# Performance work log

Measured on AMD Instinct MI355X. Metric: run time of the kernel, lower is better.

## Reference

```python
import jax, jax.numpy as jnp
from jax import lax
import numpy as np

D_MODEL, D_STATE, D_CONV, EXPAND = 512, 16, 4, 2
D_INNER = EXPAND * D_MODEL
B_SZ, SEQ = 16, 2048


def setup_inputs() -> dict:
    key = jax.random.key(0)
    ks = jax.random.split(key, 8)
    s = 0.02
    x = jax.random.normal(ks[0], (B_SZ, SEQ, D_MODEL), jnp.float32)
    W_in = jax.random.normal(ks[1], (2 * D_INNER, D_MODEL), jnp.float32) * s
    conv_w = jax.random.normal(ks[2], (D_INNER, 1, D_CONV), jnp.float32) * s
    conv_b = jnp.zeros((D_INNER,), jnp.float32)
    W_x = jax.random.normal(ks[3], (2 * D_STATE, D_INNER), jnp.float32) * s
    W_dt = jax.random.normal(ks[4], (D_INNER, D_INNER), jnp.float32) * s
    b_dt = jnp.zeros((D_INNER,), jnp.float32)
    # A_log = -logspace(log10(0.001), log10(1.0), d_state), exactly as in source
    A_log = jnp.asarray(-np.logspace(np.log10(0.001), 0.0, D_STATE), jnp.float32)
    D = jnp.ones((D_INNER,), jnp.float32) * 0.1
    W_out = jax.random.normal(ks[5], (D_MODEL, D_INNER), jnp.float32) * s
    ln_g = jnp.ones((D_MODEL,), jnp.float32)
    ln_b = jnp.zeros((D_MODEL,), jnp.float32)
    return dict(x=x, W_in=W_in, conv_w=conv_w, conv_b=conv_b, W_x=W_x,
                W_dt=W_dt, b_dt=b_dt, A_log=A_log, D=D, W_out=W_out,
                ln_g=ln_g, ln_b=ln_b)


def _selective_scan(u, delta, A, B, C, Dp):
    # u, delta: [b, s, di]; B, C: [b, s, ds]; A: [ds]; Dp: [di]
    def step(state, inp):
        d_t, u_t, B_t, C_t = inp            # [b,di],[b,di],[b,ds],[b,ds]
        dA = jnp.exp(jnp.clip(d_t[:, :, None] * A[None, None, :], -5.0, 5.0))
        dBu = (d_t * u_t)[:, :, None] * B_t[:, None, :]
        state = dA * state + dBu            # [b,di,ds]
        y_t = jnp.einsum('bds,bs->bd', state, C_t)
        return state, y_t

    b = u.shape[0]
    init = jnp.zeros((b, D_INNER, D_STATE), u.dtype)
    xs = (delta.transpose(1, 0, 2), u.transpose(1, 0, 2),
          B.transpose(1, 0, 2), C.transpose(1, 0, 2))
    _, ys = lax.scan(step, init, xs)        # [s, b, di]
    return ys.transpose(1, 0, 2) + u * Dp


def reference(x, W_in, conv_w, conv_b, W_x, W_dt, b_dt, A_log, D, W_out, ln_g, ln_b):
    x = jnp.clip(x, -10.0, 10.0)
    x_and_res = x @ W_in.T                  # [b, s, 2*di]
    x_p, res = jnp.split(x_and_res, 2, axis=-1)
    # causal depthwise conv1d (left pad d_conv-1, truncate to seq_len)
    xc = lax.conv_general_dilated(
        x_p.transpose(0, 2, 1), conv_w, window_strides=(1,),
        padding=[(D_CONV - 1, 0)], dimension_numbers=('NCH', 'OIH', 'NCH'),
        feature_group_count=D_INNER)
    xc = (xc + conv_b[None, :, None]).transpose(0, 2, 1)  # [b, s, di]
    xc = jax.nn.silu(xc)
    ssm = xc @ W_x.T                        # [b, s, 2*ds]
    Bm, Cm = jnp.split(ssm, 2, axis=-1)
    dt = xc @ W_dt.T + b_dt                 # [b, s, di]
    y = _selective_scan(xc, dt, A_log, Bm, Cm, D)
    y = y * jax.nn.silu(res)
    out = y @ W_out.T + x
    # LayerNorm (eps=1e-5)
    mu = out.mean(-1, keepdims=True)
    var = ((out - mu) ** 2).mean(-1, keepdims=True)
    return (out - mu) * lax.rsqrt(var + 1e-5) * ln_g + ln_b
```

## Files before the change

### kernel.cpp

```cpp
#include <hip/hip_runtime.h>
#include <hip/hip_bf16.h>
#include <math.h>

#define B_SZ 16
#define SEQ 2048
#define D_MODEL 512
#define D_INNER 1024
#define D_STATE 16
#define D_CONV 4
#define NSEG 64
#define SEGLEN (SEQ / NSEG)
#define LOG2E 1.44269504f

typedef __attribute__((ext_vector_type(8))) short short8;
typedef __attribute__((ext_vector_type(4))) float f32x4;
typedef const __attribute__((address_space(1))) void* gas_ptr;
typedef __attribute__((address_space(3))) void* las_ptr;

__device__ __forceinline__ float bf2f(unsigned int bits16) {
    union { unsigned int i; float f; } v; v.i = bits16 << 16; return v.f;
}
__device__ __forceinline__ unsigned short f2bf(float f) {
    union { float f; unsigned int i; } v; v.f = f;
    unsigned int r = v.i + 0x7FFFu + ((v.i >> 16) & 1u);
    return (unsigned short)(r >> 16);
}
__device__ __forceinline__ void async_g2l(const void* g, void* l) {
    __builtin_amdgcn_global_load_lds((gas_ptr)g, (las_ptr)l, 16, 0, 0);
}
__device__ __forceinline__ float fast_exp2(float x) { return __builtin_amdgcn_exp2f(x); }
__device__ __forceinline__ float fast_rcp(float x)  { return __builtin_amdgcn_rcpf(x); }
__device__ __forceinline__ float clamp3(float x, float lo, float hi) {
    return __builtin_amdgcn_fmed3f(x, lo, hi);
}
__device__ __forceinline__ float silu(float x) {
    return x * fast_rcp(1.f + fast_exp2(-x * LOG2E));
}
__device__ __forceinline__ void vm_wait0() { asm volatile("s_waitcnt vmcnt(0)" ::: "memory"); }
__device__ __forceinline__ void vm_wait3() { asm volatile("s_waitcnt vmcnt(3)" ::: "memory"); }
__device__ __forceinline__ void vm_wait4() { asm volatile("s_waitcnt vmcnt(4)" ::: "memory"); }

__global__ __launch_bounds__(256) void cast_bf16(
    const float4* __restrict__ in, ushort4* __restrict__ out, int n4, int do_clip)
{
    int i = blockIdx.x * 256 + threadIdx.x;
    if (i >= n4) return;
    float4 v = in[i];
    if (do_clip) {
        v.x = clamp3(v.x, -10.f, 10.f);
        v.y = clamp3(v.y, -10.f, 10.f);
        v.z = clamp3(v.z, -10.f, 10.f);
        v.w = clamp3(v.w, -10.f, 10.f);
    }
    ushort4 o;
    o.x = f2bf(v.x); o.y = f2bf(v.y); o.z = f2bf(v.z); o.w = f2bf(v.w);
    out[i] = o;
}

__global__ __launch_bounds__(512, 4) void gemm_big(
    const unsigned short* __restrict__ A, const unsigned short* __restrict__ Bw,
    void* __restrict__ C, int K, int ldc, int nbn_shift,
    const float* __restrict__ bias,
    const float* __restrict__ add, int ldadd, int clip_add, int out_bf16)
{
    __shared__ unsigned short As[3][256][32];
    __shared__ unsigned short Bs[3][128][32];
    const int h = blockIdx.x;
    const int xk = h & 7;
    const int qb = h >> 3;
    const int bn = (qb & ((1 << nbn_shift) - 1)) * 128;
    const int bm = ((qb >> nbn_shift) * 8 + xk) * 256;
    const int tid = threadIdx.x;
    const int wv = tid >> 6;
    const int l  = tid & 63;
    const int lr = l >> 2;
    const int lc = l & 3;
    const int wm = (wv >> 1) * 64;
    const int wn = (wv & 1) * 64;
    const int r16 = l & 15;
    const int q   = l >> 4;
    const int gsw = (lc - ((lr >> 1) & 3)) & 3;
    const int ssw = ((q + ((r16 >> 1) & 3)) & 3) * 8;

    f32x4 acc[4][4];
    #pragma unroll
    for (int i = 0; i < 4; i++)
        #pragma unroll
        for (int j = 0; j < 4; j++)
            acc[i][j] = (f32x4){0.f, 0.f, 0.f, 0.f};

#define STAGEB(kk, bb) { \
        const int k0_ = (kk) * 32; \
        _Pragma("unroll") \
        for (int p_ = 0; p_ < 2; p_++) { \
            const int arow_ = wv * 32 + p_ * 16 + lr; \
            async_g2l((const char*)A + (((size_t)(bm + arow_)) * K + k0_ + gsw * 8) * 2, \
                      (char*)&As[bb][wv * 32 + p_ * 16][0]); \
        } \
        const int brow_ = wv * 16 + lr; \
        async_g2l((const char*)Bw + (((size_t)(bn + brow_)) * K + k0_ + gsw * 8) * 2, \
                  (char*)&Bs[bb][wv * 16][0]); \
    }

    const int nk = K >> 5;
    STAGEB(0, 0);
    STAGEB(1, 1);
    int c0 = 0, c1 = 1, c2 = 2;

    for (int kk = 0; kk < nk; kk++) {
        if (kk + 1 < nk) vm_wait3(); else vm_wait0();
        __builtin_amdgcn_s_barrier();

        short8 af[4], bfv[4];
        #pragma unroll
        for (int i = 0; i < 4; i++) {
            af[i]  = *(const short8*)&As[c0][wm + i * 16 + r16][ssw];
            bfv[i] = *(const short8*)&Bs[c0][wn + i * 16 + r16][ssw];
        }
        if (kk + 2 < nk) STAGEB(kk + 2, c2);

        #pragma unroll
        for (int i = 0; i < 4; i++)
            #pragma unroll
            for (int j = 0; j < 4; j++)
                acc[i][j] = __builtin_amdgcn_mfma_f32_16x16x32_bf16(
                    af[i], bfv[j], acc[i][j], 0, 0, 0);

        int t = c0; c0 = c1; c1 = c2; c2 = t;
    }
#undef STAGEB

    #pragma unroll
    for (int i = 0; i < 4; i++) {
        #pragma unroll
        for (int rr = 0; rr < 4; rr++) {
            int m = bm + wm + i * 16 + q * 4 + rr;
            #pragma unroll
            for (int j = 0; j < 4; j++) {
                int n = bn + wn + j * 16 + r16;
                float v = acc[i][j][rr];
                if (bias) v += bias[n];
                if (add) {
                    float a = add[(size_t)m * ldadd + n];
                    if (clip_add) a = clamp3(a, -10.f, 10.f);
                    v += a;
                }
                if (out_bf16)
                    ((unsigned short*)C)[(size_t)m * ldc + n] = f2bf(v);
                else
                    ((float*)C)[(size_t)m * ldc + n] = v;
            }
        }
    }
}

__global__ __launch_bounds__(256) void gemm_bf16(
    const unsigned short* __restrict__ A, const unsigned short* __restrict__ Bw,
    void* __restrict__ C, int K, int ldc, int nbn_shift,
    const float* __restrict__ bias,
    const float* __restrict__ add, int ldadd, int clip_add, int out_bf16)
{
    __shared__ unsigned short As[3][128][32];
    __shared__ unsigned short Bs[3][128][32];
    const int h = blockIdx.x;
    const int xk = h & 7;
    const int qb = h >> 3;
    const int bn = (qb & ((1 << nbn_shift) - 1)) * 128;
    const int bm = ((qb >> nbn_shift) * 8 + xk) * 128;
    const int tid = threadIdx.x;
    const int wv = tid >> 6;
    const int l  = tid & 63;
    const int lr = l >> 2;
    const int lc = l & 3;
    const int wm = (wv >> 1) * 64;
    const int wn = (wv & 1) * 64;
    const int r16 = l & 15;
    const int q   = l >> 4;
    const int gsw = (lc - ((lr >> 1) & 3)) & 3;
    const int ssw = ((q + ((r16 >> 1) & 3)) & 3) * 8;

    f32x4 acc[4][4];
    #pragma unroll
    for (int i = 0; i < 4; i++)
        #pragma unroll
        for (int j = 0; j < 4; j++)
            acc[i][j] = (f32x4){0.f, 0.f, 0.f, 0.f};

#define STAGE(kk, bb) { \
        const int k0_ = (kk) * 32; \
        _Pragma("unroll") \
        for (int p_ = 0; p_ < 2; p_++) { \
            const int row_ = wv * 32 + p_ * 16 + lr; \
            async_g2l((const char*)A + (((size_t)(bm + row_)) * K + k0_ + gsw * 8) * 2, \
                      (char*)&As[bb][wv * 32 + p_ * 16][0]); \
            async_g2l((const char*)Bw + (((size_t)(bn + row_)) * K + k0_ + gsw * 8) * 2, \
                      (char*)&Bs[bb][wv * 32 + p_ * 16][0]); \
        } }

    const int nk = K >> 5;
    STAGE(0, 0);
    STAGE(1, 1);
    int c0 = 0, c1 = 1, c2 = 2;

    for (int kk = 0; kk < nk; kk++) {
        if (kk + 1 < nk) vm_wait4(); else vm_wait0();
        __builtin_amdgcn_s_barrier();

        short8 af[4], bfv[4];
        #pragma unroll
        for (int i = 0; i < 4; i++) {
            af[i]  = *(const short8*)&As[c0][wm + i * 16 + r16][ssw];
            bfv[i] = *(const short8*)&Bs[c0][wn + i * 16 + r16][ssw];
        }
        if (kk + 2 < nk) STAGE(kk + 2, c2);

        #pragma unroll
        for (int i = 0; i < 4; i++)
            #pragma unroll
            for (int j = 0; j < 4; j++)
                acc[i][j] = __builtin_amdgcn_mfma_f32_16x16x32_bf16(
                    af[i], bfv[j], acc[i][j], 0, 0, 0);

        int t = c0; c0 = c1; c1 = c2; c2 = t;
    }
#undef STAGE

    #pragma unroll
    for (int i = 0; i < 4; i++) {
        #pragma unroll
        for (int rr = 0; rr < 4; rr++) {
            int m = bm + wm + i * 16 + q * 4 + rr;
            #pragma unroll
            for (int j = 0; j < 4; j++) {
                int n = bn + wn + j * 16 + r16;
                float v = acc[i][j][rr];
                if (bias) v += bias[n];
                if (add) {
                    float a = add[(size_t)m * ldadd + n];
                    if (clip_add) a = clamp3(a, -10.f, 10.f);
                    v += a;
                }
                if (out_bf16)
                    ((unsigned short*)C)[(size_t)m * ldc + n] = f2bf(v);
                else
                    ((float*)C)[(size_t)m * ldc + n] = v;
            }
        }
    }
}

__global__ __launch_bounds__(256) void gemm_bc(
    const unsigned short* __restrict__ A, const unsigned short* __restrict__ Bw,
    float* __restrict__ C)
{
    const int tid = threadIdx.x;
    const int wv  = tid >> 6;
    const int l   = tid & 63;
    const int r16 = l & 15;
    const int q   = l >> 4;
    const int row0 = blockIdx.x * 64 + wv * 16;

    const unsigned short* ap  = A  + (size_t)(row0 + r16) * 1024 + q * 8;
    const unsigned short* bp0 = Bw + (size_t)r16 * 1024 + q * 8;
    const unsigned short* bp1 = Bw + (size_t)(16 + r16) * 1024 + q * 8;

    f32x4 acc0 = {0.f, 0.f, 0.f, 0.f}, acc1 = {0.f, 0.f, 0.f, 0.f};
    #pragma unroll 4
    for (int k = 0; k < 1024; k += 32) {
        short8 af = *(const short8*)(ap + k);
        short8 b0 = *(const short8*)(bp0 + k);
        short8 b1 = *(const short8*)(bp1 + k);
        acc0 = __builtin_amdgcn_mfma_f32_16x16x32_bf16(af, b0, acc0, 0, 0, 0);
        acc1 = __builtin_amdgcn_mfma_f32_16x16x32_bf16(af, b1, acc1, 0, 0, 0);
    }
    #pragma unroll
    for (int rr = 0; rr < 4; rr++) {
        int m = row0 + q * 4 + rr;
        C[(size_t)m * 32 + r16]      = acc0[rr];
        C[(size_t)m * 32 + 16 + r16] = acc1[rr];
    }
}

__global__ __launch_bounds__(256) void conv_silu(
    const unsigned short* __restrict__ xp, const float* __restrict__ cw,
    const float* __restrict__ cb, unsigned short* __restrict__ xc)
{
    int idx = blockIdx.x * 256 + threadIdx.x;
    int c4 = (idx & 255) << 2;
    int bt = idx >> 8;
    int t  = bt & (SEQ - 1);

    float4 acc = *(const float4*)(cb + c4);
    float4 w0 = *(const float4*)(cw + (c4 + 0) * 4);
    float4 w1 = *(const float4*)(cw + (c4 + 1) * 4);
    float4 w2 = *(const float4*)(cw + (c4 + 2) * 4);
    float4 w3 = *(const float4*)(cw + (c4 + 3) * 4);

    #pragma unroll
    for (int k = 0; k < D_CONV; k++) {
        int tt = t - (D_CONV - 1) + k;
        if (tt >= 0) {
            ushort4 xv = *(const ushort4*)(xp + (size_t)(bt - (D_CONV - 1) + k) * 2048 + c4);
            acc.x += bf2f(xv.x) * ((const float*)&w0)[k];
            acc.y += bf2f(xv.y) * ((const float*)&w1)[k];
            acc.z += bf2f(xv.z) * ((const float*)&w2)[k];
            acc.w += bf2f(xv.w) * ((const float*)&w3)[k];
        }
    }
    ushort4 o;
    o.x = f2bf(silu(acc.x));
    o.y = f2bf(silu(acc.y));
    o.z = f2bf(silu(acc.z));
    o.w = f2bf(silu(acc.w));
    *(ushort4*)(xc + (size_t)bt * 1024 + c4) = o;
}

__global__ __launch_bounds__(64, 4) void scan_phaseA(
    const unsigned short* __restrict__ xpres, const float* __restrict__ BC,
    const unsigned short* __restrict__ xc, const float* __restrict__ A_log,
    float* __restrict__ stA, float* __restrict__ prA)
{
    __shared__ float bc_lds[SEGLEN][32];
    const int bx = blockIdx.x;
    const int seg = bx & (NSEG - 1);
    const int dg  = (bx >> 6) & 15;
    const int b   = bx >> 10;
    if (seg == NSEG - 1) return;
    const int lane = threadIdx.x;
    const int d = dg * 64 + lane;
    const float CL = 5.f * LOG2E;

    const size_t rowbase = (size_t)b * SEQ + (size_t)seg * SEGLEN;
    const float* BCp = BC + rowbase * 32;

    #pragma unroll
    for (int c = 0; c < 4; c++)
        async_g2l(BCp + c * 256 + lane * 4,
                  (char*)&bc_lds[0][0] + c * 1024 + lane * 16);

    float A2[16];
    #pragma unroll
    for (int n = 0; n < 16; n++) A2[n] = A_log[n] * LOG2E;

    const unsigned short* dtp = xpres + rowbase * 2048 + d;
    const unsigned short* up  = xc + rowbase * 1024 + d;

    float st[16] = {};
    float se[16] = {};
    unsigned short dta[4], dtb[4], ua[4], ub[4];

#define LOADGA(g, dt_, u_) { \
        _Pragma("unroll") for (int jj = 0; jj < 4; ++jj) { \
            const int t_ = (g) * 4 + jj; \
            dt_[jj] = dtp[(size_t)t_ * 2048]; \
            u_[jj]  = up[(size_t)t_ * 1024]; \
        } }

#define COMPGA(g, dt_, u_) { \
        _Pragma("unroll") for (int jj = 0; jj < 4; ++jj) { \
            const int t_ = (g) * 4 + jj; \
            const float dtv_ = bf2f(dt_[jj]); \
            const float du_ = dtv_ * bf2f(u_[jj]); \
            float Bv_[16]; \
            _Pragma("unroll") for (int n = 0; n < 4; ++n) \
                *(float4*)&Bv_[n * 4] = *(const float4*)&bc_lds[t_][n * 4]; \
            _Pragma("unroll") for (int n = 0; n < 16; ++n) { \
                const float e_ = clamp3(dtv_ * A2[n], -CL, CL); \
                se[n] += e_; \
                st[n] = fast_exp2(e_) * st[n] + du_ * Bv_[n]; \
            } } }

    LOADGA(0, dta, ua);
    __syncthreads();

    for (int g = 0; g < 8; g += 2) {
        LOADGA(g + 1, dtb, ub);
        COMPGA(g, dta, ua);
        if (g + 2 < 8) LOADGA(g + 2, dta, ua);
        COMPGA(g + 1, dtb, ub);
    }
#undef LOADGA
#undef COMPGA

    size_t o = (((size_t)b * NSEG + seg) * 1024 + d) * 16;
    #pragma unroll
    for (int n4 = 0; n4 < 4; n4++) {
        *(float4*)(stA + o + n4 * 4) = *(float4*)&st[n4 * 4];
        float4 pv;
        pv.x = fast_exp2(clamp3(se[n4 * 4 + 0], -115.41f, 115.41f));
        pv.y = fast_exp2(clamp3(se[n4 * 4 + 1], -115.41f, 115.41f));
        pv.z = fast_exp2(clamp3(se[n4 * 4 + 2], -115.41f, 115.41f));
        pv.w = fast_exp2(clamp3(se[n4 * 4 + 3], -115.41f, 115.41f));
        *(float4*)(prA + o + n4 * 4) = pv;
    }
}

__global__ __launch_bounds__(256) void scan_combine(
    float* __restrict__ stA, const float* __restrict__ prA, int total)
{
    int idx = blockIdx.x * 256 + threadIdx.x;
    if (idx >= total) return;
    int dn = idx & 16383;
    int b  = idx >> 14;
    float prev = 0.f;
    #pragma unroll 4
    for (int s = 0; s < NSEG; s++) {
        size_t o = ((size_t)b * NSEG + s) * 16384 + dn;
        float a = stA[o], pr = prA[o];
        stA[o] = prev;
        prev = a + pr * prev;
    }
}

__global__ __launch_bounds__(64, 4) void scan_phaseC(
    const unsigned short* __restrict__ xpres, const float* __restrict__ BC,
    const unsigned short* __restrict__ xc, const float* __restrict__ A_log,
    const float* __restrict__ Dvec, const float* __restrict__ stIn,
    unsigned short* __restrict__ y_bf)
{
    __shared__ float bc_lds[SEGLEN][32];
    const int bx = blockIdx.x;
    const int seg = bx & (NSEG - 1);
    const int dg  = (bx >> 6) & 15;
    const int b   = bx >> 10;
    const int lane = threadIdx.x;
    const int d = dg * 64 + lane;
    const float CL = 5.f * LOG2E;

    const size_t rowbase = (size_t)b * SEQ + (size_t)seg * SEGLEN;
    const float* BCp = BC + rowbase * 32;

    #pragma unroll
    for (int c = 0; c < 4; c++)
        async_g2l(BCp + c * 256 + lane * 4,
                  (char*)&bc_lds[0][0] + c * 1024 + lane * 16);

    float A2[16];
    #pragma unroll
    for (int n = 0; n < 16; n++) A2[n] = A_log[n] * LOG2E;
    const float Dp = Dvec[d];

    const unsigned short* dtp  = xpres + rowbase * 2048 + d;
    const unsigned short* resp = xpres + rowbase * 2048 + 1024 + d;
    const unsigned short* up   = xc + rowbase * 1024 + d;
    unsigned short* yp = y_bf + rowbase * 1024 + d;

    float st[16];
    size_t o = (((size_t)b * NSEG + seg) * 1024 + d) * 16;
    #pragma unroll
    for (int n4 = 0; n4 < 4; n4++)
        *(float4*)&st[n4 * 4] = *(const float4*)(stIn + o + n4 * 4);

    unsigned short dta[4], dtb[4], ua[4], ub[4], ra[4], rb[4];

#define LOADGC(g, dt_, r_, u_) { \
        _Pragma("unroll") for (int jj = 0; jj < 4; ++jj) { \
            const int t_ = (g) * 4 + jj; \
            dt_[jj] = dtp[(size_t)t_ * 2048]; \
            r_[jj]  = resp[(size_t)t_ * 2048]; \
            u_[jj]  = up[(size_t)t_ * 1024]; \
        } }

#define COMPGC(g, dt_, r_, u_) { \
        _Pragma("unroll") for (int jj = 0; jj < 4; ++jj) { \
            const int t_ = (g) * 4 + jj; \
            const float dtv_ = bf2f(dt_[jj]); \
            const float uu_ = bf2f(u_[jj]); \
            const float du_ = dtv_ * uu_; \
            float V_[16]; \
            _Pragma("unroll") for (int n = 0; n < 4; ++n) \
                *(float4*)&V_[n * 4] = *(const float4*)&bc_lds[t_][n * 4]; \
            _Pragma("unroll") for (int n = 0; n < 16; ++n) { \
                const float e_ = clamp3(dtv_ * A2[n], -CL, CL); \
                st[n] = fast_exp2(e_) * st[n] + du_ * V_[n]; \
            } \
            _Pragma("unroll") for (int n = 0; n < 4; ++n) \
                *(float4*)&V_[n * 4] = *(const float4*)&bc_lds[t_][16 + n * 4]; \
            float y_ = 0.f; \
            _Pragma("unroll") for (int n = 0; n < 16; ++n) \
                y_ += st[n] * V_[n]; \
            const float outv_ = (y_ + uu_ * Dp) * silu(bf2f(r_[jj])); \
            yp[(size_t)t_ * 1024] = f2bf(outv_); \
        } }

    LOADGC(0, dta, ra, ua);
    __syncthreads();

    for (int g = 0; g < 8; g += 2) {
        LOADGC(g + 1, dtb, rb, ub);
        COMPGC(g, dta, ra, ua);
        if (g + 2 < 8) LOADGC(g + 2, dta, ra, ua);
        COMPGC(g + 1, dtb, rb, ub);
    }
#undef LOADGC
#undef COMPGC
}

__global__ __launch_bounds__(128) void ln_kernel(
    float* __restrict__ out, const float* __restrict__ g,
    const float* __restrict__ bta)
{
    const int row = blockIdx.x;
    float* p = out + (size_t)row * D_MODEL;
    const int tid = threadIdx.x;

    float4 v = ((const float4*)p)[tid];
    float s1 = v.x + v.y + v.z + v.w;
    float s2 = v.x * v.x + v.y * v.y + v.z * v.z + v.w * v.w;
    #pragma unroll
    for (int off = 32; off > 0; off >>= 1) {
        s1 += __shfl_xor(s1, off);
        s2 += __shfl_xor(s2, off);
    }
    __shared__ float r1[2], r2[2];
    if ((tid & 63) == 0) { r1[tid >> 6] = s1; r2[tid >> 6] = s2; }
    __syncthreads();
    s1 = r1[0] + r1[1];
    s2 = r2[0] + r2[1];

    const float mu  = s1 * (1.f / D_MODEL);
    const float var = s2 * (1.f / D_MODEL) - mu * mu;
    const float rstd = rsqrtf(var + 1e-5f);

    float4 gg = ((const float4*)g)[tid];
    float4 bb = ((const float4*)bta)[tid];
    float4 o;
    o.x = (v.x - mu) * rstd * gg.x + bb.x;
    o.y = (v.y - mu) * rstd * gg.y + bb.y;
    o.z = (v.z - mu) * rstd * gg.z + bb.z;
    o.w = (v.w - mu) * rstd * gg.w + bb.w;
    ((float4*)p)[tid] = o;
}

extern "C" void kernel_launch(void* const* d_in, const int* in_sizes, int n_in,
                              void* d_out, int out_size, void* d_ws, size_t ws_size,
                              hipStream_t stream)
{
    const float* x      = (const float*)d_in[0];
    const float* W_in   = (const float*)d_in[1];
    const float* conv_w = (const float*)d_in[2];
    const float* conv_b = (const float*)d_in[3];
    const float* W_x    = (const float*)d_in[4];
    const float* W_dt   = (const float*)d_in[5];
    const float* b_dt   = (const float*)d_in[6];
    const float* A_log  = (const float*)d_in[7];
    const float* Dv     = (const float*)d_in[8];
    const float* W_out  = (const float*)d_in[9];
    const float* ln_g   = (const float*)d_in[10];
    const float* ln_b   = (const float*)d_in[11];
    float* out = (float*)d_out;

    const size_t szWin  = (size_t)2048 * 512;
    const size_t szWdt  = (size_t)1024 * 1024;
    const size_t szWout = (size_t)512 * 1024;
    const size_t szWx   = (size_t)32 * 1024;
    char* p = (char*)d_ws;
    unsigned short* Wib  = (unsigned short*)p; p += szWin * 2;
    unsigned short* Wdtb = (unsigned short*)p; p += szWdt * 2;
    unsigned short* Wob  = (unsigned short*)p; p += szWout * 2;
    unsigned short* Wxb  = (unsigned short*)p; p += szWx * 2;
    const size_t fixed_bytes = (size_t)(p - (char*)d_ws);

    const size_t per_batch =
        (size_t)SEQ * 2048 * 2
      + (size_t)SEQ * 1024 * 2
      + (size_t)SEQ * 1024 * 2
      + (size_t)SEQ * 32 * 4
      + (size_t)2 * NSEG * 1024 * 16 * 4;
    int cb = 16;
    while (cb > 1 && fixed_bytes + (size_t)cb * per_batch > ws_size) cb >>= 1;
    const int Mc = cb * SEQ;

    unsigned short* xpres = (unsigned short*)p; p += (size_t)Mc * 2048 * 2;
    unsigned short* ybuf  = (unsigned short*)p; p += (size_t)Mc * 1024 * 2;
    unsigned short* x_bf  = ybuf;
    unsigned short* xc_bf = (unsigned short*)p; p += (size_t)Mc * 1024 * 2;
    float*          BCb   = (float*)p;          p += (size_t)Mc * 32 * 4;
    float*          stA   = (float*)p;          p += (size_t)cb * NSEG * 16384 * 4;
    float*          prA   = (float*)p;

    cast_bf16<<<(int)(szWin / 4 + 255) / 256, 256, 0, stream>>>((const float4*)W_in,  (ushort4*)Wib,  (int)(szWin / 4), 0);
    cast_bf16<<<(int)(szWdt / 4 + 255) / 256, 256, 0, stream>>>((const float4*)W_dt,  (ushort4*)Wdtb, (int)(szWdt / 4), 0);
    cast_bf16<<<(int)(szWout / 4 + 255) / 256, 256, 0, stream>>>((const float4*)W_out, (ushort4*)Wob, (int)(szWout / 4), 0);
    cast_bf16<<<(int)(szWx / 4 + 255) / 256, 256, 0, stream>>>((const float4*)W_x,   (ushort4*)Wxb,  (int)(szWx / 4), 0);

    for (int b0 = 0; b0 < B_SZ; b0 += cb) {
        const float* xk   = x   + (size_t)b0 * SEQ * D_MODEL;
        float*       outk = out + (size_t)b0 * SEQ * D_MODEL;

        cast_bf16<<<(Mc * 512 / 4) / 256, 256, 0, stream>>>(
            (const float4*)xk, (ushort4*)x_bf, Mc * 512 / 4, 1);

        gemm_big<<<16 * (Mc / 256), 512, 0, stream>>>(
            x_bf, Wib, xpres, 512, 2048, 4, nullptr, nullptr, 0, 0, 1);

        conv_silu<<<Mc, 256, 0, stream>>>(xpres, conv_w, conv_b, xc_bf);

        gemm_bc<<<Mc / 64, 256, 0, stream>>>(xc_bf, Wxb, BCb);

        gemm_big<<<8 * (Mc / 256), 512, 0, stream>>>(
            xc_bf, Wdtb, xpres, 1024, 2048, 3, b_dt, nullptr, 0, 0, 1);

        scan_phaseA<<<cb * NSEG * 16, 64, 0, stream>>>(xpres, BCb, xc_bf, A_log, stA, prA);
        scan_combine<<<(cb * 16384 + 255) / 256, 256, 0, stream>>>(stA, prA, cb * 16384);
        scan_phaseC<<<cb * NSEG * 16, 64, 0, stream>>>(xpres, BCb, xc_bf, A_log, Dv, stA, ybuf);

        gemm_bf16<<<4 * (Mc / 128), 256, 0, stream>>>(
            ybuf, Wob, outk, 1024, 512, 2, nullptr, xk, 512, 1, 0);

        ln_kernel<<<Mc, 128, 0, stream>>>(outk, ln_g, ln_b);
    }
}
```

Before: 875.8 us.

## Split scan state dimension across two half-waves per channel

The scan phase A and C kernels now use 128 threads per block, and each channel's 16 SSM states are split across two 32-lane halves of a wave, each holding 8 states. Phase C combines the partial y outputs with a cross-half shuffle, and only the first half writes the result. This halves per-thread register state and serial work while doubling thread-level parallelism. The cost is redundant dt/u loads and exp work per channel, half-wave divergence on the store, and less coalesced 32-lane global accesses.

```diff
diff --git a/kernel.cpp b/kernel.cpp
--- a/kernel.cpp
+++ b/kernel.cpp
@@ -315,7 +315,7 @@
     *(ushort4*)(xc + (size_t)bt * 1024 + c4) = o;
 }
 
-__global__ __launch_bounds__(64, 4) void scan_phaseA(
+__global__ __launch_bounds__(128, 8) void scan_phaseA(
     const unsigned short* __restrict__ xpres, const float* __restrict__ BC,
     const unsigned short* __restrict__ xc, const float* __restrict__ A_log,
     float* __restrict__ stA, float* __restrict__ prA)
@@ -326,27 +326,31 @@
     const int dg  = (bx >> 6) & 15;
     const int b   = bx >> 10;
     if (seg == NSEG - 1) return;
-    const int lane = threadIdx.x;
-    const int d = dg * 64 + lane;
+    const int tid  = threadIdx.x;
+    const int wv   = tid >> 6;
+    const int half = (tid >> 5) & 1;
+    const int dl   = tid & 31;
+    const int d    = dg * 64 + wv * 32 + dl;
+    const int n0   = half * 8;
     const float CL = 5.f * LOG2E;
 
     const size_t rowbase = (size_t)b * SEQ + (size_t)seg * SEGLEN;
     const float* BCp = BC + rowbase * 32;
 
     #pragma unroll
-    for (int c = 0; c < 4; c++)
-        async_g2l(BCp + c * 256 + lane * 4,
-                  (char*)&bc_lds[0][0] + c * 1024 + lane * 16);
-
-    float A2[16];
-    #pragma unroll
-    for (int n = 0; n < 16; n++) A2[n] = A_log[n] * LOG2E;
+    for (int c = 0; c < 2; c++)
+        async_g2l(BCp + c * 512 + tid * 4,
+                  (char*)&bc_lds[0][0] + c * 2048 + tid * 16);
+
+    float A2[8];
+    #pragma unroll
+    for (int n = 0; n < 8; n++) A2[n] = A_log[n0 + n] * LOG2E;
 
     const unsigned short* dtp = xpres + rowbase * 2048 + d;
     const unsigned short* up  = xc + rowbase * 1024 + d;
 
-    float st[16] = {};
-    float se[16] = {};
+    float st[8] = {};
+    float se[8] = {};
     unsigned short dta[4], dtb[4], ua[4], ub[4];
 
 #define LOADGA(g, dt_, u_) { \
@@ -361,10 +365,10 @@
             const int t_ = (g) * 4 + jj; \
             const float dtv_ = bf2f(dt_[jj]); \
             const float du_ = dtv_ * bf2f(u_[jj]); \
-            float Bv_[16]; \
-            _Pragma("unroll") for (int n = 0; n < 4; ++n) \
-                *(float4*)&Bv_[n * 4] = *(const float4*)&bc_lds[t_][n * 4]; \
-            _Pragma("unroll") for (int n = 0; n < 16; ++n) { \
+            float Bv_[8]; \
+            *(float4*)&Bv_[0] = *(const float4*)&bc_lds[t_][n0]; \
+            *(float4*)&Bv_[4] = *(const float4*)&bc_lds[t_][n0 + 4]; \
+            _Pragma("unroll") for (int n = 0; n < 8; ++n) { \
                 const float e_ = clamp3(dtv_ * A2[n], -CL, CL); \
                 se[n] += e_; \
                 st[n] = fast_exp2(e_) * st[n] + du_ * Bv_[n]; \
@@ -382,17 +386,20 @@
 #undef LOADGA
 #undef COMPGA
 
-    size_t o = (((size_t)b * NSEG + seg) * 1024 + d) * 16;
-    #pragma unroll
-    for (int n4 = 0; n4 < 4; n4++) {
-        *(float4*)(stA + o + n4 * 4) = *(float4*)&st[n4 * 4];
-        float4 pv;
-        pv.x = fast_exp2(clamp3(se[n4 * 4 + 0], -115.41f, 115.41f));
-        pv.y = fast_exp2(clamp3(se[n4 * 4 + 1], -115.41f, 115.41f));
-        pv.z = fast_exp2(clamp3(se[n4 * 4 + 2], -115.41f, 115.41f));
-        pv.w = fast_exp2(clamp3(se[n4 * 4 + 3], -115.41f, 115.41f));
-        *(float4*)(prA + o + n4 * 4) = pv;
-    }
+    size_t o = (((size_t)b * NSEG + seg) * 1024 + d) * 16 + n0;
+    *(float4*)(stA + o)     = *(float4*)&st[0];
+    *(float4*)(stA + o + 4) = *(float4*)&st[4];
+    float4 p0, p1;
+    p0.x = fast_exp2(clamp3(se[0], -115.41f, 115.41f));
+    p0.y = fast_exp2(clamp3(se[1], -115.41f, 115.41f));
+    p0.z = fast_exp2(clamp3(se[2], -115.41f, 115.41f));
+    p0.w = fast_exp2(clamp3(se[3], -115.41f, 115.41f));
+    p1.x = fast_exp2(clamp3(se[4], -115.41f, 115.41f));
+    p1.y = fast_exp2(clamp3(se[5], -115.41f, 115.41f));
+    p1.z = fast_exp2(clamp3(se[6], -115.41f, 115.41f));
+    p1.w = fast_exp2(clamp3(se[7], -115.41f, 115.41f));
+    *(float4*)(prA + o)     = p0;
+    *(float4*)(prA + o + 4) = p1;
 }
 
 __global__ __launch_bounds__(256) void scan_combine(
@@ -412,7 +419,7 @@
     }
 }
 
-__global__ __launch_bounds__(64, 4) void scan_phaseC(
+__global__ __launch_bounds__(128, 8) void scan_phaseC(
     const unsigned short* __restrict__ xpres, const float* __restrict__ BC,
     const unsigned short* __restrict__ xc, const float* __restrict__ A_log,
     const float* __restrict__ Dvec, const float* __restrict__ stIn,
@@ -423,21 +430,25 @@
     const int seg = bx & (NSEG - 1);
     const int dg  = (bx >> 6) & 15;
     const int b   = bx >> 10;
-    const int lane = threadIdx.x;
-    const int d = dg * 64 + lane;
+    const int tid  = threadIdx.x;
+    const int wv   = tid >> 6;
+    const int half = (tid >> 5) & 1;
+    const int dl   = tid & 31;
+    const int d    = dg * 64 + wv * 32 + dl;
+    const int n0   = half * 8;
     const float CL = 5.f * LOG2E;
 
     const size_t rowbase = (size_t)b * SEQ + (size_t)seg * SEGLEN;
     const float* BCp = BC + rowbase * 32;
 
     #pragma unroll
-    for (int c = 0; c < 4; c++)
-        async_g2l(BCp + c * 256 + lane * 4,
-                  (char*)&bc_lds[0][0] + c * 1024 + lane * 16);
-
-    float A2[16];
-    #pragma unroll
-    for (int n = 0; n < 16; n++) A2[n] = A_log[n] * LOG2E;
+    for (int c = 0; c < 2; c++)
+        async_g2l(BCp + c * 512 + tid * 4,
+                  (char*)&bc_lds[0][0] + c * 2048 + tid * 16);
+
+    float A2[8];
+    #pragma unroll
+    for (int n = 0; n < 8; n++) A2[n] = A_log[n0 + n] * LOG2E;
     const float Dp = Dvec[d];
 
     const unsigned short* dtp  = xpres + rowbase * 2048 + d;
@@ -445,11 +456,10 @@
     const unsigned short* up   = xc + rowbase * 1024 + d;
     unsigned short* yp = y_bf + rowbase * 1024 + d;
 
-    float st[16];
-    size_t o = (((size_t)b * NSEG + seg) * 1024 + d) * 16;
-    #pragma unroll
-    for (int n4 = 0; n4 < 4; n4++)
-        *(float4*)&st[n4 * 4] = *(const float4*)(stIn + o + n4 * 4);
+    float st[8];
+    size_t o = (((size_t)b * NSEG + seg) * 1024 + d) * 16 + n0;
+    *(float4*)&st[0] = *(const float4*)(stIn + o);
+    *(float4*)&st[4] = *(const float4*)(stIn + o + 4);
 
     unsigned short dta[4], dtb[4], ua[4], ub[4], ra[4], rb[4];
 
@@ -467,21 +477,23 @@
             const float dtv_ = bf2f(dt_[jj]); \
             const float uu_ = bf2f(u_[jj]); \
             const float du_ = dtv_ * uu_; \
-            float V_[16]; \
-            _Pragma("unroll") for (int n = 0; n < 4; ++n) \
-                *(float4*)&V_[n * 4] = *(const float4*)&bc_lds[t_][n * 4]; \
-            _Pragma("unroll") for (int n = 0; n < 16; ++n) { \
+            float V_[8]; \
+            *(float4*)&V_[0] = *(const float4*)&bc_lds[t_][n0]; \
+            *(float4*)&V_[4] = *(const float4*)&bc_lds[t_][n0 + 4]; \
+            _Pragma("unroll") for (int n = 0; n < 8; ++n) { \
                 const float e_ = clamp3(dtv_ * A2[n], -CL, CL); \
                 st[n] = fast_exp2(e_) * st[n] + du_ * V_[n]; \
             } \
-            _Pragma("unroll") for (int n = 0; n < 4; ++n) \
-                *(float4*)&V_[n * 4] = *(const float4*)&bc_lds[t_][16 + n * 4]; \
+            *(float4*)&V_[0] = *(const float4*)&bc_lds[t_][16 + n0]; \
+            *(float4*)&V_[4] = *(const float4*)&bc_lds[t_][16 + n0 + 4]; \
             float y_ = 0.f; \
-            _Pragma("unroll") for (int n = 0; n < 16; ++n) \
+            _Pragma("unroll") for (int n = 0; n < 8; ++n) \
                 y_ += st[n] * V_[n]; \
-            const float outv_ = (y_ + uu_ * Dp) * silu(bf2f(r_[jj])); \
-            yp[(size_t)t_ * 1024] = f2bf(outv_); \
-        } }
+            y_ += __shfl_xor(y_, 32); \
+            if (half == 0) { \
+                const float outv_ = (y_ + uu_ * Dp) * silu(bf2f(r_[jj])); \
+                yp[(size_t)t_ * 1024] = f2bf(outv_); \
+            } } }
 
     LOADGC(0, dta, ra, ua);
     __syncthreads();
@@ -601,9 +613,9 @@
         gemm_big<<<8 * (Mc / 256), 512, 0, stream>>>(
             xc_bf, Wdtb, xpres, 1024, 2048, 3, b_dt, nullptr, 0, 0, 1);
 
-        scan_phaseA<<<cb * NSEG * 16, 64, 0, stream>>>(xpres, BCb, xc_bf, A_log, stA, prA);
+        scan_phaseA<<<cb * NSEG * 16, 128, 0, stream>>>(xpres, BCb, xc_bf, A_log, stA, prA);
         scan_combine<<<(cb * 16384 + 255) / 256, 256, 0, stream>>>(stA, prA, cb * 16384);
-        scan_phaseC<<<cb * NSEG * 16, 64, 0, stream>>>(xpres, BCb, xc_bf, A_log, Dv, stA, ybuf);
+        scan_phaseC<<<cb * NSEG * 16, 128, 0, stream>>>(xpres, BCb, xc_bf, A_log, Dv, stA, ybuf);
 
         gemm_bf16<<<4 * (Mc / 128), 256, 0, stream>>>(
             ybuf, Wob, outk, 1024, 512, 2, nullptr, xk, 512, 1, 0);
```

Result: slower. 1.437 ms (+64.1%).
